# Optimization experiments

Measured on AMD Instinct MI355X. Metric: run time of the kernel, lower is better.

The kernel has to match this reference:

```python
import jax, jax.numpy as jnp
import numpy as np

N_NODES = 100000

def setup_inputs() -> dict:
    key = jax.random.key(0)
    k1, k2, k3 = jax.random.split(key, 3)
    x = jax.random.normal(k1, (N_NODES, 64), dtype=jnp.float32)
    edge_index = jax.random.randint(k2, (2, 1250000), 0, N_NODES, dtype=jnp.int64)
    edge_weight = jax.random.uniform(k3, (1250000,), dtype=jnp.float32)
    return {"x": x, "edge_index": edge_index, "edge_weight": edge_weight}

def reference(x, edge_index, edge_weight):
    # LightGCNConv: out[dst] = sum_e edge_weight[e] * x[src_e]  (aggr='add')
    src, dst = edge_index[0], edge_index[1]
    msgs = edge_weight[:, None] * x[src]          # [E, d] gather-multiply
    out = jax.ops.segment_sum(msgs, dst, num_segments=N_NODES)  # scatter-add
    return out
```

## Files before the change

### kernel.cpp

```cpp
#include <hip/hip_runtime.h>
#include <hip/hip_bf16.h>


#define N_NODES   100000
#define N_FEAT    64

#define A_BSH     7
#define A_NPB     (1 << A_BSH)
#define A_KB      ((N_NODES + A_NPB - 1) >> A_BSH)
#define A_CAP     2048
#define A_FCHUNK  4096
#define A_OVCAP   65536
#define NBIN      ((1250000 + A_FCHUNK - 1) / A_FCHUNK)
#define NCAST     391

__global__ __launch_bounds__(1024) void k_castbin(
    const float* __restrict__ x, ushort* __restrict__ xb,
    const int* __restrict__ ei, const float* __restrict__ w,
    int* __restrict__ bcur, int2* __restrict__ stg,
    int* __restrict__ ovf, int* __restrict__ ovcnt, int E) {
    int t = threadIdx.x;
    if (blockIdx.x >= NBIN) {
        int cb = blockIdx.x - NBIN;
        #pragma unroll
        for (int k = 0; k < 4; ++k) {
            int i4 = cb * 4096 + k * 1024 + t;
            if (i4 < N_NODES * N_FEAT / 4) {
                float4 v = ((const float4*)x)[i4];
                uint4 u = *(uint4*)&v;
                ushort4 r;
                r.x = (ushort)((u.x + 0x7FFFu + ((u.x >> 16) & 1)) >> 16);
                r.y = (ushort)((u.y + 0x7FFFu + ((u.y >> 16) & 1)) >> 16);
                r.z = (ushort)((u.z + 0x7FFFu + ((u.z >> 16) & 1)) >> 16);
                r.w = (ushort)((u.w + 0x7FFFu + ((u.w >> 16) & 1)) >> 16);
                ((ushort4*)xb)[i4] = r;
            }
        }
        return;
    }
    __shared__ int h[A_KB];
    for (int b = t; b < A_KB; b += 1024) h[b] = 0;
    __syncthreads();
    int e0 = blockIdx.x * A_FCHUNK;
    int dstv[A_FCHUNK / 1024];
    int srcv[A_FCHUNK / 1024];
    float wv[A_FCHUNK / 1024];
    #pragma unroll
    for (int k = 0; k < A_FCHUNK / 1024; ++k) {
        int e = e0 + k * 1024 + t;
        bool ok = (e < E);
        dstv[k] = ok ? ei[E + e] : -1;
        srcv[k] = ok ? ei[e] : 0;
        wv[k]   = ok ? w[e] : 0.f;
        if (ok) atomicAdd(&h[dstv[k] >> A_BSH], 1);
    }
    __syncthreads();
    for (int b = t; b < A_KB; b += 1024) {
        int c = h[b];
        h[b] = c ? atomicAdd(&bcur[b], c) : 0;
    }
    __syncthreads();
    #pragma unroll
    for (int k = 0; k < A_FCHUNK / 1024; ++k) {
        if (dstv[k] >= 0) {
            int b = dstv[k] >> A_BSH;
            int loc = atomicAdd(&h[b], 1);
            if (loc < A_CAP) {
                stg[b * A_CAP + loc] =
                    make_int2(srcv[k] | ((dstv[k] & (A_NPB - 1)) << 17),
                              __float_as_int(wv[k]));
            } else {
                int oi = atomicAdd(ovcnt, 1);
                if (oi < A_OVCAP) ovf[oi] = e0 + k * 1024 + t;
            }
        }
    }
}

__global__ __launch_bounds__(1024) void k_sortgather(
    const ushort* __restrict__ xb, const int* __restrict__ bcur,
    const int2* __restrict__ stg, float* __restrict__ out) {
    __shared__ int2 buf[A_CAP];
    __shared__ int2 srt[A_CAP];
    __shared__ int  hist[A_NPB];
    __shared__ int  start[A_NPB];
    __shared__ int  cur[A_NPB];
    int b = blockIdx.x, t = threadIdx.x;
    int cnt = bcur[b];
    if (cnt > A_CAP) cnt = A_CAP;
    int base = b * A_CAP;

    if (t < A_NPB) hist[t] = 0;
    __syncthreads();
    for (int i = t; i < cnt; i += 1024) {
        int2 p = stg[base + i];
        buf[i] = p;
        atomicAdd(&hist[(p.x >> 17) & (A_NPB - 1)], 1);
    }
    __syncthreads();
    if (t < A_NPB) cur[t] = hist[t];
    __syncthreads();
    for (int off = 1; off < A_NPB; off <<= 1) {
        int v = (t < A_NPB && t >= off) ? cur[t - off] : 0;
        __syncthreads();
        if (t < A_NPB && t >= off) cur[t] += v;
        __syncthreads();
    }
    if (t < A_NPB) start[t] = (t == 0) ? 0 : cur[t - 1];
    __syncthreads();
    if (t < A_NPB) cur[t] = start[t];
    __syncthreads();
    for (int i = t; i < cnt; i += 1024) {
        int2 p = buf[i];
        int pos = atomicAdd(&cur[(p.x >> 17) & (A_NPB - 1)], 1);
        srt[pos] = p;
    }
    __syncthreads();

    int wid  = t >> 6;
    int lane = t & 63;
    int q    = lane >> 4;
    int l    = lane & 15;
    const ushort4* xb4 = (const ushort4*)xb;
    #pragma unroll
    for (int pass = 0; pass < 2; ++pass) {
        int n = pass * 64 + wid * 4 + q;
        int node = (b << A_BSH) + n;
        int j = start[n], end = start[n] + hist[n];
        float ax0 = 0.f, ay0 = 0.f, az0 = 0.f, aw0 = 0.f;
        float ax1 = 0.f, ay1 = 0.f, az1 = 0.f, aw1 = 0.f;
        for (; j + 1 < end; j += 2) {
            int2 p0 = srt[j];
            int2 p1 = srt[j + 1];
            ushort4 u0 = xb4[(size_t)(p0.x & 0x1FFFF) * 16 + l];
            ushort4 u1 = xb4[(size_t)(p1.x & 0x1FFFF) * 16 + l];
            float w0 = __int_as_float(p0.y), w1 = __int_as_float(p1.y);
            ax0 += w0 * __uint_as_float((uint)u0.x << 16);
            ay0 += w0 * __uint_as_float((uint)u0.y << 16);
            az0 += w0 * __uint_as_float((uint)u0.z << 16);
            aw0 += w0 * __uint_as_float((uint)u0.w << 16);
            ax1 += w1 * __uint_as_float((uint)u1.x << 16);
            ay1 += w1 * __uint_as_float((uint)u1.y << 16);
            az1 += w1 * __uint_as_float((uint)u1.z << 16);
            aw1 += w1 * __uint_as_float((uint)u1.w << 16);
        }
        if (j < end) {
            int2 p = srt[j];
            ushort4 u = xb4[(size_t)(p.x & 0x1FFFF) * 16 + l];
            float wv = __int_as_float(p.y);
            ax0 += wv * __uint_as_float((uint)u.x << 16);
            ay0 += wv * __uint_as_float((uint)u.y << 16);
            az0 += wv * __uint_as_float((uint)u.z << 16);
            aw0 += wv * __uint_as_float((uint)u.w << 16);
        }
        if (node < N_NODES) {
            float4 r;
            r.x = ax0 + ax1; r.y = ay0 + ay1;
            r.z = az0 + az1; r.w = aw0 + aw1;
            ((float4*)out)[(size_t)node * 16 + l] = r;
        }
    }
}

__global__ __launch_bounds__(256) void k_ovf(
    const float* __restrict__ x, const int* __restrict__ ei,
    const float* __restrict__ w, const int* __restrict__ ovf,
    const int* __restrict__ ovcnt, float* __restrict__ out, int E) {
    int n = *ovcnt;
    if (n > A_OVCAP) n = A_OVCAP;
    int wid  = blockIdx.x * 4 + (threadIdx.x >> 6);
    int lane = threadIdx.x & 63;
    for (int i = wid; i < n; i += gridDim.x * 4) {
        int e = ovf[i];
        float v = w[e] * x[(size_t)ei[e] * N_FEAT + lane];
        atomicAdd(&out[(size_t)ei[E + e] * N_FEAT + lane], v);
    }
}

#define BSH       8
#define NPB       (1 << BSH)
#define KB        ((N_NODES + NPB - 1) >> BSH)
#define FCHUNK    8192
#define SORT_CAP  4096

__global__ __launch_bounds__(256) void k_chist(
    const int* __restrict__ ei, int* __restrict__ bcur, int E) {
    __shared__ int h[KB];
    int t = threadIdx.x;
    for (int b = t; b < KB; b += 256) h[b] = 0;
    __syncthreads();
    int e0 = blockIdx.x * FCHUNK;
    #pragma unroll
    for (int k = 0; k < FCHUNK / 256; ++k) {
        int e = e0 + k * 256 + t;
        if (e < E) atomicAdd(&h[ei[E + e] >> BSH], 1);
    }
    __syncthreads();
    for (int b = t; b < KB; b += 256) if (h[b]) atomicAdd(&bcur[b], h[b]);
}

__global__ __launch_bounds__(256) void k_cscan(
    int* __restrict__ bcur, int* __restrict__ boffs) {
    __shared__ int sdata[256];
    int t = threadIdx.x;
    int i0 = 2 * t, i1 = 2 * t + 1;
    int v0 = (i0 < KB) ? bcur[i0] : 0;
    int v1 = (i1 < KB) ? bcur[i1] : 0;
    sdata[t] = v0 + v1; __syncthreads();
    for (int off = 1; off < 256; off <<= 1) {
        int v = (t >= off) ? sdata[t - off] : 0;
        __syncthreads();
        if (t >= off) sdata[t] += v;
        __syncthreads();
    }
    int run = (t == 0) ? 0 : sdata[t - 1];
    if (i0 < KB) { boffs[i0] = run; bcur[i0] = run; }
    run += v0;
    if (i1 < KB) { boffs[i1] = run; bcur[i1] = run; }
    if (t == 255) boffs[KB] = sdata[255];
}

__global__ __launch_bounds__(256) void k_cbin(
    const int* __restrict__ ei, const float* __restrict__ w,
    int* __restrict__ bcur, int2* __restrict__ stg, int E) {
    __shared__ int h[KB];
    int t = threadIdx.x;
    for (int b = t; b < KB; b += 256) h[b] = 0;
    __syncthreads();
    int e0 = blockIdx.x * FCHUNK;
    #pragma unroll
    for (int k = 0; k < FCHUNK / 256; ++k) {
        int e = e0 + k * 256 + t;
        if (e < E) atomicAdd(&h[ei[E + e] >> BSH], 1);
    }
    __syncthreads();
    for (int b = t; b < KB; b += 256) {
        int c = h[b];
        h[b] = c ? atomicAdd(&bcur[b], c) : 0;
    }
    __syncthreads();
    #pragma unroll
    for (int k = 0; k < FCHUNK / 256; ++k) {
        int e = e0 + k * 256 + t;
        if (e < E) {
            int dst = ei[E + e];
            int slot = atomicAdd(&h[dst >> BSH], 1);
            stg[slot] = make_int2(ei[e] | ((dst & (NPB - 1)) << 17),
                                  __float_as_int(w[e]));
        }
    }
}

__global__ __launch_bounds__(256) void k_csort(
    int2* __restrict__ stg, const int* __restrict__ boffs,
    int* __restrict__ offs) {
    __shared__ int2 buf[SORT_CAP];
    __shared__ int  hist[NPB];
    __shared__ int  cur[NPB];
    __shared__ int  sdata[256];
    int b = blockIdx.x, t = threadIdx.x;
    int bg = boffs[b], end = boffs[b + 1], cnt = end - bg;
    for (int n = t; n < NPB; n += 256) hist[n] = 0;
    __syncthreads();
    int nlds = cnt < SORT_CAP ? cnt : SORT_CAP;
    for (int i = t; i < nlds; i += 256) {
        int2 p = stg[bg + i];
        buf[i] = p;
        atomicAdd(&hist[(p.x >> 17) & (NPB - 1)], 1);
    }
    int2 r0{0,0}, r1{0,0}; int nr = 0;
    {
        int i0 = nlds + t, i1 = nlds + 256 + t;
        if (i0 < cnt) { r0 = stg[bg + i0]; atomicAdd(&hist[(r0.x >> 17) & (NPB - 1)], 1); nr = 1; }
        if (i1 < cnt) { r1 = stg[bg + i1]; atomicAdd(&hist[(r1.x >> 17) & (NPB - 1)], 1); nr = 2; }
    }
    __syncthreads();
    int c = hist[t];
    sdata[t] = c; __syncthreads();
    for (int off = 1; off < 256; off <<= 1) {
        int v = (t >= off) ? sdata[t - off] : 0;
        __syncthreads();
        if (t >= off) sdata[t] += v;
        __syncthreads();
    }
    int excl = (t == 0) ? 0 : sdata[t - 1];
    cur[t] = excl;
    int node = (b << BSH) + t;
    if (node < N_NODES) offs[node] = bg + excl;
    if (b == KB - 1 && t == 255) offs[N_NODES] = end;
    __syncthreads();
    for (int i = t; i < nlds; i += 256) {
        int2 p = buf[i];
        int pos = atomicAdd(&cur[(p.x >> 17) & (NPB - 1)], 1);
        stg[bg + pos] = p;
    }
    if (nr >= 1) { int pos = atomicAdd(&cur[(r0.x >> 17) & (NPB - 1)], 1); stg[bg + pos] = r0; }
    if (nr >= 2) { int pos = atomicAdd(&cur[(r1.x >> 17) & (NPB - 1)], 1); stg[bg + pos] = r1; }
}

__global__ __launch_bounds__(256) void k_gather(
    const float* __restrict__ x, const int* __restrict__ offs,
    const int2* __restrict__ stg, float* __restrict__ out) {
    int node = blockIdx.x * 4 + (threadIdx.x >> 6);
    int lane = threadIdx.x & 63;
    if (node >= N_NODES) return;
    int bg = offs[node], end = offs[node + 1];
    float a0 = 0.f, a1 = 0.f, a2 = 0.f, a3 = 0.f;
    int j = bg;
    for (; j + 3 < end; j += 4) {
        int2 p0 = stg[j];
        int2 p1 = stg[j + 1];
        int2 p2 = stg[j + 2];
        int2 p3 = stg[j + 3];
        a0 += __int_as_float(p0.y) * x[(size_t)(p0.x & 0x1FFFF) * N_FEAT + lane];
        a1 += __int_as_float(p1.y) * x[(size_t)(p1.x & 0x1FFFF) * N_FEAT + lane];
        a2 += __int_as_float(p2.y) * x[(size_t)(p2.x & 0x1FFFF) * N_FEAT + lane];
        a3 += __int_as_float(p3.y) * x[(size_t)(p3.x & 0x1FFFF) * N_FEAT + lane];
    }
    for (; j < end; ++j) {
        int2 p = stg[j];
        a0 += __int_as_float(p.y) * x[(size_t)(p.x & 0x1FFFF) * N_FEAT + lane];
    }
    out[(size_t)node * N_FEAT + lane] = (a0 + a1) + (a2 + a3);
}

__global__ __launch_bounds__(256) void gnn_scatter_kernel(
    const float* __restrict__ x, const int* __restrict__ ei,
    const float* __restrict__ w, float* __restrict__ out, int E) {
    int e = blockIdx.x * 4 + (threadIdx.x >> 6);
    int lane = threadIdx.x & 63;
    if (e >= E) return;
    float v = w[e] * x[(size_t)ei[e] * N_FEAT + lane];
    atomicAdd(&out[(size_t)ei[E + e] * N_FEAT + lane], v);
}

static inline size_t align16(size_t v) { return (v + 15) & ~(size_t)15; }

extern "C" void kernel_launch(void* const* d_in, const int* in_sizes, int n_in,
                              void* d_out, int out_size, void* d_ws, size_t ws_size,
                              hipStream_t stream) {
    const float* x   = (const float*)d_in[0];
    const int*   ei  = (const int*)d_in[1];
    const float* w   = (const float*)d_in[2];
    float*       out = (float*)d_out;
    const int E = in_sizes[2];
    char* ws = (char*)d_ws;

    size_t a_xb   = 0;
    size_t a_stg  = align16(a_xb + (size_t)N_NODES * N_FEAT * 2);
    size_t a_bcur = align16(a_stg + (size_t)A_KB * A_CAP * 8);
    size_t a_ovf  = align16(a_bcur + (size_t)(A_KB + 1) * 4);
    size_t need_a = a_ovf + (size_t)A_OVCAP * 4;

    if (ws_size >= need_a && E == 1250000) {
        ushort* xb    = (ushort*)(ws + a_xb);
        int2*   stg   = (int2*)(ws + a_stg);
        int*    bcur  = (int*)(ws + a_bcur);
        int*    ovcnt = bcur + A_KB;
        int*    ovf   = (int*)(ws + a_ovf);

        hipMemsetAsync(bcur, 0, (size_t)(A_KB + 1) * 4, stream);
        k_castbin<<<NBIN + NCAST, 1024, 0, stream>>>(
            x, xb, ei, w, bcur, stg, ovf, ovcnt, E);
        k_sortgather<<<A_KB, 1024, 0, stream>>>(xb, bcur, stg, out);
        k_ovf<<<16, 256, 0, stream>>>(x, ei, w, ovf, ovcnt, out, E);
        return;
    }

    size_t b_bcur  = 0;
    size_t b_boffs = align16(b_bcur + (size_t)KB * 4);
    size_t b_offs  = align16(b_boffs + (size_t)(KB + 1) * 4);
    size_t b_stg   = align16(b_offs + (size_t)(N_NODES + 1) * 4);
    size_t need_b  = b_stg + (size_t)E * 8;

    if (ws_size >= need_b) {
        int*  bcur  = (int*)(ws + b_bcur);
        int*  boffs = (int*)(ws + b_boffs);
        int*  offs  = (int*)(ws + b_offs);
        int2* stg   = (int2*)(ws + b_stg);
        const int nblk = (E + FCHUNK - 1) / FCHUNK;
        hipMemsetAsync(bcur, 0, (size_t)KB * 4, stream);
        k_chist<<<nblk, 256, 0, stream>>>(ei, bcur, E);
        k_cscan<<<1, 256, 0, stream>>>(bcur, boffs);
        k_cbin<<<nblk, 256, 0, stream>>>(ei, w, bcur, stg, E);
        k_csort<<<KB, 256, 0, stream>>>(stg, boffs, offs);
        k_gather<<<(N_NODES + 3) / 4, 256, 0, stream>>>(x, offs, stg, out);
        return;
    }

    hipMemsetAsync(d_out, 0, (size_t)out_size * sizeof(float), stream);
    gnn_scatter_kernel<<<(E + 3) / 4, 256, 0, stream>>>(x, ei, w, out, E);
}
```

Measured before the change: 136.4 us.

## Fold overflow edges into sortgather, shrink block to 512, use wave-shuffle scan

Removes the separate overflow kernel and instead has each node's accumulating lanes scan the overflow list and add matching edges before the single store, so there are no global atomics and one fewer launch. The sortgather block shrinks from 1024 to 512 threads with four node passes instead of two, and the 128-entry shared-memory Hillis-Steele scan is replaced by a single-wave shuffle scan over pairs. The overflow scan is linear in the overflow count per node pass, which could be costly if overflow is non-trivial. With random inputs it is likely near zero.

```diff
diff --git a/kernel.cpp b/kernel.cpp
--- a/kernel.cpp
+++ b/kernel.cpp
@@ -77,40 +77,46 @@
     }
 }
 
-__global__ __launch_bounds__(1024) void k_sortgather(
+__global__ __launch_bounds__(512, 8) void k_sortgather(
     const ushort* __restrict__ xb, const int* __restrict__ bcur,
-    const int2* __restrict__ stg, float* __restrict__ out) {
+    const int2* __restrict__ stg, float* __restrict__ out,
+    const float* __restrict__ x, const int* __restrict__ ei,
+    const float* __restrict__ w, const int* __restrict__ ovf,
+    const int* __restrict__ ovcnt, int E) {
     __shared__ int2 buf[A_CAP];
     __shared__ int2 srt[A_CAP];
     __shared__ int  hist[A_NPB];
     __shared__ int  start[A_NPB];
     __shared__ int  cur[A_NPB];
+    __shared__ int  ovn;
     int b = blockIdx.x, t = threadIdx.x;
     int cnt = bcur[b];
     if (cnt > A_CAP) cnt = A_CAP;
     int base = b * A_CAP;
 
     if (t < A_NPB) hist[t] = 0;
-    __syncthreads();
-    for (int i = t; i < cnt; i += 1024) {
+    if (t == 0) { int n = *ovcnt; ovn = (n > A_OVCAP) ? A_OVCAP : n; }
+    __syncthreads();
+    for (int i = t; i < cnt; i += 512) {
         int2 p = stg[base + i];
         buf[i] = p;
         atomicAdd(&hist[(p.x >> 17) & (A_NPB - 1)], 1);
     }
     __syncthreads();
-    if (t < A_NPB) cur[t] = hist[t];
-    __syncthreads();
-    for (int off = 1; off < A_NPB; off <<= 1) {
-        int v = (t < A_NPB && t >= off) ? cur[t - off] : 0;
-        __syncthreads();
-        if (t < A_NPB && t >= off) cur[t] += v;
-        __syncthreads();
-    }
-    if (t < A_NPB) start[t] = (t == 0) ? 0 : cur[t - 1];
-    __syncthreads();
-    if (t < A_NPB) cur[t] = start[t];
-    __syncthreads();
-    for (int i = t; i < cnt; i += 1024) {
+    if (t < 64) {
+        int s0 = hist[2 * t], s1 = hist[2 * t + 1];
+        int ps = s0 + s1;
+        #pragma unroll
+        for (int off = 1; off < 64; off <<= 1) {
+            int v = __shfl_up(ps, off);
+            if (t >= off) ps += v;
+        }
+        int excl = ps - (s0 + s1);
+        start[2 * t]     = excl;       cur[2 * t]     = excl;
+        start[2 * t + 1] = excl + s0;  cur[2 * t + 1] = excl + s0;
+    }
+    __syncthreads();
+    for (int i = t; i < cnt; i += 512) {
         int2 p = buf[i];
         int pos = atomicAdd(&cur[(p.x >> 17) & (A_NPB - 1)], 1);
         srt[pos] = p;
@@ -122,9 +128,10 @@
     int q    = lane >> 4;
     int l    = lane & 15;
     const ushort4* xb4 = (const ushort4*)xb;
-    #pragma unroll
-    for (int pass = 0; pass < 2; ++pass) {
-        int n = pass * 64 + wid * 4 + q;
+    int novf = ovn;
+    #pragma unroll
+    for (int pass = 0; pass < 4; ++pass) {
+        int n = pass * 32 + wid * 4 + q;
         int node = (b << A_BSH) + n;
         int j = start[n], end = start[n] + hist[n];
         float ax0 = 0.f, ay0 = 0.f, az0 = 0.f, aw0 = 0.f;
@@ -153,27 +160,23 @@
             az0 += wv * __uint_as_float((uint)u.z << 16);
             aw0 += wv * __uint_as_float((uint)u.w << 16);
         }
+        if (novf) {
+            for (int i = 0; i < novf; ++i) {
+                int e = ovf[i];
+                if (ei[E + e] == node) {
+                    float wv = w[e];
+                    float4 xv = ((const float4*)x)[(size_t)ei[e] * 16 + l];
+                    ax0 += wv * xv.x; ay0 += wv * xv.y;
+                    az0 += wv * xv.z; aw0 += wv * xv.w;
+                }
+            }
+        }
         if (node < N_NODES) {
             float4 r;
             r.x = ax0 + ax1; r.y = ay0 + ay1;
             r.z = az0 + az1; r.w = aw0 + aw1;
             ((float4*)out)[(size_t)node * 16 + l] = r;
         }
-    }
-}
-
-__global__ __launch_bounds__(256) void k_ovf(
-    const float* __restrict__ x, const int* __restrict__ ei,
-    const float* __restrict__ w, const int* __restrict__ ovf,
-    const int* __restrict__ ovcnt, float* __restrict__ out, int E) {
-    int n = *ovcnt;
-    if (n > A_OVCAP) n = A_OVCAP;
-    int wid  = blockIdx.x * 4 + (threadIdx.x >> 6);
-    int lane = threadIdx.x & 63;
-    for (int i = wid; i < n; i += gridDim.x * 4) {
-        int e = ovf[i];
-        float v = w[e] * x[(size_t)ei[e] * N_FEAT + lane];
-        atomicAdd(&out[(size_t)ei[E + e] * N_FEAT + lane], v);
     }
 }
 
@@ -362,8 +365,8 @@
         hipMemsetAsync(bcur, 0, (size_t)(A_KB + 1) * 4, stream);
         k_castbin<<<NBIN + NCAST, 1024, 0, stream>>>(
             x, xb, ei, w, bcur, stg, ovf, ovcnt, E);
-        k_sortgather<<<A_KB, 1024, 0, stream>>>(xb, bcur, stg, out);
-        k_ovf<<<16, 256, 0, stream>>>(x, ei, w, ovf, ovcnt, out, E);
+        k_sortgather<<<A_KB, 512, 0, stream>>>(
+            xb, bcur, stg, out, x, ei, w, ovf, ovcnt, E);
         return;
     }
 
```

Measured after the change: 131.4 us. 3.7% less time.
